# Optimization experiments

Measured on AMD Instinct MI355X. Metric: run time of the kernel, lower is better.

## Reference

```python
import jax, jax.numpy as jnp
import numpy as np

NX, NY = 8192, 8192
C1, C2, D = 2048, 2048, 512

def setup_inputs() -> dict:
    key = jax.random.key(0)
    k1, k2, k3, k4, k5 = jax.random.split(key, 5)
    scale1 = 1.0 / np.sqrt(C1)
    scale2 = 1.0 / np.sqrt(C2)
    return {
        "x": jax.random.normal(k1, (NX, C1), dtype=jnp.float32),
        "y": jax.random.normal(k2, (NY, C2), dtype=jnp.float32),
        "Wq": jax.random.uniform(k3, (D, C1), dtype=jnp.float32, minval=-scale1, maxval=scale1),
        "Wk": jax.random.uniform(k4, (D, C2), dtype=jnp.float32, minval=-scale2, maxval=scale2),
        "Wv": jax.random.uniform(k5, (D, C2), dtype=jnp.float32, minval=-scale2, maxval=scale2),
    }

def reference(x, y, Wq, Wk, Wv):
    d = Wq.shape[0]
    q = x @ Wq.T                      # [nx, d]
    k = y @ Wk.T                      # [ny, d]
    v = y @ Wv.T                      # [ny, d]
    a = (q @ k.T) * (d ** -0.5)       # [nx, ny]
    # torch.triu(ones) masks upper triangle INCLUDING diagonal -> zero where j >= i
    nx, ny = a.shape
    i = jnp.arange(nx)[:, None]
    j = jnp.arange(ny)[None, :]
    a = jnp.where(j >= i, 0.0, a)
    return a @ v                      # [nx, d]
```

## Files before the change

### kernel.cpp

```cpp
#include <hip/hip_runtime.h>
#include <hip/hip_bf16.h>


typedef __bf16 bf16x8 __attribute__((ext_vector_type(8)));
typedef __bf16 bf16x4 __attribute__((ext_vector_type(4)));
typedef float f32x4 __attribute__((ext_vector_type(4)));

#define MFMA16(a, b, c) __builtin_amdgcn_mfma_f32_16x16x32_bf16(a, b, c, 0, 0, 0)

constexpr float SCALE = 0.04419417382415922f;

__device__ __forceinline__ void ld16(const void* g, void* l) {
    __builtin_amdgcn_global_load_lds(
        (__attribute__((address_space(1))) void*)g,
        (__attribute__((address_space(3))) void*)l, 16, 0, 0);
}

__device__ __forceinline__ bf16x8 frag(const __bf16* base, int r, int c) {
    return *(const bf16x8*)((const char*)base + r * 128 + ((c ^ (r & 7)) * 16));
}

__device__ inline bf16x8 pack8(float4 a, float4 b) {
    bf16x8 r;
    r[0] = (__bf16)a.x; r[1] = (__bf16)a.y; r[2] = (__bf16)a.z; r[3] = (__bf16)a.w;
    r[4] = (__bf16)b.x; r[5] = (__bf16)b.y; r[6] = (__bf16)b.z; r[7] = (__bf16)b.w;
    return r;
}

__global__ __launch_bounds__(256) void convert_all(
    const float* __restrict__ x, const float* __restrict__ y,
    const float* __restrict__ wqf, const float* __restrict__ wkf,
    const float* __restrict__ wvf, __bf16* __restrict__ xb,
    __bf16* __restrict__ yb, __bf16* __restrict__ wqb,
    __bf16* __restrict__ wkb, __bf16* __restrict__ wvb)
{
    size_t uid = (size_t)blockIdx.x * 256 + threadIdx.x;
    const float* src; __bf16* dst; size_t off;
    if (uid < 2097152)      { src = x;   dst = xb;  off = uid; }
    else if (uid < 4194304) { src = y;   dst = yb;  off = uid - 2097152; }
    else if (uid < 4325376) { src = wqf; dst = wqb; off = uid - 4194304; }
    else if (uid < 4456448) { src = wkf; dst = wkb; off = uid - 4325376; }
    else                    { src = wvf; dst = wvb; off = uid - 4456448; }
    float4 a = ((const float4*)src)[off * 2];
    float4 b = ((const float4*)src)[off * 2 + 1];
    *(bf16x8*)(dst + off * 8) = pack8(a, b);
}

__global__ __launch_bounds__(256, 3) void gemm_qkv_bf16(
    const __bf16* __restrict__ xb, const __bf16* __restrict__ yb,
    const __bf16* __restrict__ wq, const __bf16* __restrict__ wk,
    const __bf16* __restrict__ wv, __bf16* __restrict__ qo,
    __bf16* __restrict__ ko, __bf16* __restrict__ vo)
{
    constexpr int K = 2048, N = 512;
    __shared__ __align__(16) __bf16 As[128][64];
    __shared__ __align__(16) __bf16 Bs[128][64];

    const int z = blockIdx.z;
    const __bf16* A = (z == 0) ? xb : yb;
    const __bf16* B = (z == 0) ? wq : (z == 1) ? wk : wv;
    __bf16* C = (z == 0) ? qo : (z == 1) ? ko : vo;
    const float mul = (z == 0) ? SCALE : 1.0f;

    const int tid  = threadIdx.x;
    const int wave = tid >> 6, lane = tid & 63;
    const int fr = lane & 15, fq = lane >> 4;
    const int m0 = blockIdx.x * 128, n0 = blockIdx.y * 128;
    const int wr = (wave >> 1) * 64, wc = (wave & 1) * 64;
    const int lr = lane >> 3;
    const int cd = (lane & 7) ^ lr;

    f32x4 acc[4][4];
#pragma unroll
    for (int a = 0; a < 4; ++a)
#pragma unroll
        for (int b = 0; b < 4; ++b) acc[a][b] = f32x4{0.f, 0.f, 0.f, 0.f};

    const __bf16* ag = A + (size_t)(m0 + wave * 32 + lr) * K + cd * 8;
    const __bf16* bg = B + (size_t)(n0 + wave * 32 + lr) * K + cd * 8;
    __bf16* al = &As[wave * 32][0];
    __bf16* bl = &Bs[wave * 32][0];

    for (int kk = 0; kk < K; kk += 64) {
        __syncthreads();
#pragma unroll
        for (int u = 0; u < 4; ++u) {
            ld16(ag + (size_t)(u * 8) * K + kk, al + u * 512);
            ld16(bg + (size_t)(u * 8) * K + kk, bl + u * 512);
        }
        __syncthreads();
#pragma unroll
        for (int ks = 0; ks < 2; ++ks) {
            bf16x8 af[4], bf[4];
#pragma unroll
            for (int rt = 0; rt < 4; ++rt)
                af[rt] = frag(&As[0][0], wr + rt * 16 + fr, ks * 4 + fq);
#pragma unroll
            for (int nt = 0; nt < 4; ++nt)
                bf[nt] = frag(&Bs[0][0], wc + nt * 16 + fr, ks * 4 + fq);
#pragma unroll
            for (int rt = 0; rt < 4; ++rt)
#pragma unroll
                for (int nt = 0; nt < 4; ++nt)
                    acc[rt][nt] = MFMA16(af[rt], bf[nt], acc[rt][nt]);
        }
    }

#pragma unroll
    for (int rt = 0; rt < 4; ++rt)
#pragma unroll
        for (int nt = 0; nt < 4; ++nt) {
            const int col = n0 + wc + nt * 16 + fr;
#pragma unroll
            for (int r = 0; r < 4; ++r) {
                const int row = m0 + wr + rt * 16 + fq * 4 + r;
                C[(size_t)row * N + col] = (__bf16)(acc[rt][nt][r] * mul);
            }
        }
}

__global__ __launch_bounds__(256) void transpose_v(
    const ushort* __restrict__ v, ushort* __restrict__ vT)
{
    __shared__ ushort tile[64][72];
    const int t = threadIdx.x;
    const int r0 = blockIdx.x * 64;
    const int c0 = blockIdx.y * 64;
    const int lr = t >> 2;
    const int lc = (t & 3) * 16;

    union { float4 f[2]; ushort s[16]; } u;
    const float4* vp = (const float4*)(v + (size_t)(r0 + lr) * 512 + c0 + lc);
    u.f[0] = vp[0];
    u.f[1] = vp[1];
#pragma unroll
    for (int e = 0; e < 16; ++e) tile[lc + e][lr] = u.s[e];
    __syncthreads();
    float4* op = (float4*)(vT + (size_t)(c0 + lr) * 8192 + r0 + lc);
    op[0] = *(const float4*)&tile[lr][lc];
    op[1] = *(const float4*)&tile[lr][lc + 8];
}

__global__ __launch_bounds__(256, 3) void h_gemm(
    const __bf16* __restrict__ vT, const __bf16* __restrict__ kT,
    __bf16* __restrict__ Ht)
{
    __shared__ __align__(16) __bf16 As[128][64];
    __shared__ __align__(16) __bf16 Bs[128][64];

    const int c  = blockIdx.y;
    const int m0 = (blockIdx.x & 3) * 128;
    const int n0 = (blockIdx.x >> 2) * 128;

    const int tid  = threadIdx.x;
    const int wave = tid >> 6, lane = tid & 63;
    const int fr = lane & 15, fq = lane >> 4;
    const int wr = (wave >> 1) * 64, wc = (wave & 1) * 64;
    const int lr = lane >> 3;
    const int cd = (lane & 7) ^ lr;

    f32x4 acc[4][4];
#pragma unroll
    for (int a = 0; a < 4; ++a)
#pragma unroll
        for (int b = 0; b < 4; ++b) acc[a][b] = f32x4{0.f, 0.f, 0.f, 0.f};

    const __bf16* ag = vT + (size_t)(m0 + wave * 32 + lr) * 8192 + c * 128 + cd * 8;
    const __bf16* bg = kT + (size_t)(n0 + wave * 32 + lr) * 8192 + c * 128 + cd * 8;
    __bf16* al = &As[wave * 32][0];
    __bf16* bl = &Bs[wave * 32][0];

    for (int kk = 0; kk < 128; kk += 64) {
        __syncthreads();
#pragma unroll
        for (int u = 0; u < 4; ++u) {
            ld16(ag + (size_t)(u * 8) * 8192 + kk, al + u * 512);
            ld16(bg + (size_t)(u * 8) * 8192 + kk, bl + u * 512);
        }
        __syncthreads();
#pragma unroll
        for (int ks = 0; ks < 2; ++ks) {
            bf16x8 af[4], bf[4];
#pragma unroll
            for (int rt = 0; rt < 4; ++rt)
                af[rt] = frag(&As[0][0], wr + rt * 16 + fr, ks * 4 + fq);
#pragma unroll
            for (int nt = 0; nt < 4; ++nt)
                bf[nt] = frag(&Bs[0][0], wc + nt * 16 + fr, ks * 4 + fq);
#pragma unroll
            for (int rt = 0; rt < 4; ++rt)
#pragma unroll
                for (int nt = 0; nt < 4; ++nt)
                    acc[rt][nt] = MFMA16(af[rt], bf[nt], acc[rt][nt]);
        }
    }

    __bf16* tp = Ht + (size_t)c * 262144;
#pragma unroll
    for (int rt = 0; rt < 4; ++rt)
#pragma unroll
        for (int nt = 0; nt < 4; ++nt) {
            const int col = n0 + wc + nt * 16 + fr;
#pragma unroll
            for (int r = 0; r < 4; ++r) {
                const int row = m0 + wr + rt * 16 + fq * 4 + r;
                tp[(size_t)row * 512 + col] = (__bf16)acc[rt][nt][r];
            }
        }
}

__global__ __launch_bounds__(256) void prefix_scan(
    const __bf16* __restrict__ Ht, __bf16* __restrict__ Pt)
{
    const size_t e = ((size_t)blockIdx.x * 256 + threadIdx.x) * 4;
    float a0 = 0.f, a1 = 0.f, a2 = 0.f, a3 = 0.f;
#pragma unroll 7
    for (int c = 0; c < 63; ++c) {
        bf16x4 h = *(const bf16x4*)(Ht + (size_t)c * 262144 + e);
        a0 += (float)h[0]; a1 += (float)h[1];
        a2 += (float)h[2]; a3 += (float)h[3];
        bf16x4 p;
        p[0] = (__bf16)a0; p[1] = (__bf16)a1;
        p[2] = (__bf16)a2; p[3] = (__bf16)a3;
        *(bf16x4*)(Pt + (size_t)(c + 1) * 262144 + e) = p;
    }
}

__global__ __launch_bounds__(256) void out_gemm(
    const __bf16* __restrict__ q, const __bf16* __restrict__ k,
    const __bf16* __restrict__ vT, const __bf16* __restrict__ Pt,
    float* __restrict__ out)
{
    __shared__ __align__(16) __bf16 As[128][64];
    __shared__ __align__(16) __bf16 Bs[128][64];
    __shared__ __align__(16) __bf16 Ss[128][136];

    const int t  = blockIdx.x;
    const int n0 = blockIdx.y * 128;

    const int tid  = threadIdx.x;
    const int wave = tid >> 6, lane = tid & 63;
    const int fr = lane & 15, fq = lane >> 4;
    const int wr = (wave >> 1) * 64, wc = (wave & 1) * 64;
    const int lr = lane >> 3;
    const int cd = (lane & 7) ^ lr;

    f32x4 acc[4][4];
#pragma unroll
    for (int a = 0; a < 4; ++a)
#pragma unroll
        for (int b = 0; b < 4; ++b) acc[a][b] = f32x4{0.f, 0.f, 0.f, 0.f};

    const __bf16* ag = q + (size_t)(t * 128 + wave * 32 + lr) * 512 + cd * 8;
    const __bf16* bg = k + (size_t)(t * 128 + wave * 32 + lr) * 512 + cd * 8;
    __bf16* al = &As[wave * 32][0];
    __bf16* bl = &Bs[wave * 32][0];

    for (int kk = 0; kk < 512; kk += 64) {
        __syncthreads();
#pragma unroll
        for (int u = 0; u < 4; ++u) {
            ld16(ag + (size_t)(u * 8) * 512 + kk, al + u * 512);
            ld16(bg + (size_t)(u * 8) * 512 + kk, bl + u * 512);
        }
        __syncthreads();
#pragma unroll
        for (int ks = 0; ks < 2; ++ks) {
            bf16x8 af[4], bf[4];
#pragma unroll
            for (int rt = 0; rt < 4; ++rt)
                af[rt] = frag(&As[0][0], wr + rt * 16 + fr, ks * 4 + fq);
#pragma unroll
            for (int nt = 0; nt < 4; ++nt)
                bf[nt] = frag(&Bs[0][0], wc + nt * 16 + fr, ks * 4 + fq);
#pragma unroll
            for (int rt = 0; rt < 4; ++rt)
#pragma unroll
                for (int nt = 0; nt < 4; ++nt)
                    acc[rt][nt] = MFMA16(af[rt], bf[nt], acc[rt][nt]);
        }
    }

#pragma unroll
    for (int rt = 0; rt < 4; ++rt)
#pragma unroll
        for (int nt = 0; nt < 4; ++nt) {
            const int col = wc + nt * 16 + fr;
#pragma unroll
            for (int r = 0; r < 4; ++r) {
                const int row = wr + rt * 16 + fq * 4 + r;
                float vv = (col < row) ? acc[rt][nt][r] : 0.f;
                Ss[row][col] = (__bf16)vv;
            }
            acc[rt][nt] = f32x4{0.f, 0.f, 0.f, 0.f};
        }

    if (t > 0) {
        const __bf16* bg2 = Pt + (size_t)t * 262144
                          + (size_t)(n0 + wave * 32 + lr) * 512 + cd * 8;
        for (int kk = 0; kk < 512; kk += 64) {
            __syncthreads();
#pragma unroll
            for (int u = 0; u < 4; ++u) {
                ld16(ag + (size_t)(u * 8) * 512 + kk, al + u * 512);
                ld16(bg2 + (size_t)(u * 8) * 512 + kk, bl + u * 512);
            }
            __syncthreads();
#pragma unroll
            for (int ks = 0; ks < 2; ++ks) {
                bf16x8 af[4], bf[4];
#pragma unroll
                for (int rt = 0; rt < 4; ++rt)
                    af[rt] = frag(&As[0][0], wr + rt * 16 + fr, ks * 4 + fq);
#pragma unroll
                for (int nt = 0; nt < 4; ++nt)
                    bf[nt] = frag(&Bs[0][0], wc + nt * 16 + fr, ks * 4 + fq);
#pragma unroll
                for (int rt = 0; rt < 4; ++rt)
#pragma unroll
                    for (int nt = 0; nt < 4; ++nt)
                        acc[rt][nt] = MFMA16(af[rt], bf[nt], acc[rt][nt]);
            }
        }
    }

    const __bf16* bg3 = vT + (size_t)(n0 + wave * 32 + lr) * 8192
                      + t * 128 + cd * 8;
    for (int kk = 0; kk < 128; kk += 64) {
        __syncthreads();
#pragma unroll
        for (int u = 0; u < 4; ++u)
            ld16(bg3 + (size_t)(u * 8) * 8192 + kk, bl + u * 512);
        __syncthreads();
#pragma unroll
        for (int ks = 0; ks < 2; ++ks) {
            bf16x8 af[4], bf[4];
#pragma unroll
            for (int rt = 0; rt < 4; ++rt)
                af[rt] = *(const bf16x8*)(&Ss[wr + rt * 16 + fr]
                                            [kk + ks * 32 + fq * 8]);
#pragma unroll
            for (int nt = 0; nt < 4; ++nt)
                bf[nt] = frag(&Bs[0][0], wc + nt * 16 + fr, ks * 4 + fq);
#pragma unroll
            for (int rt = 0; rt < 4; ++rt)
#pragma unroll
                for (int nt = 0; nt < 4; ++nt)
                    acc[rt][nt] = MFMA16(af[rt], bf[nt], acc[rt][nt]);
        }
    }

#pragma unroll
    for (int rt = 0; rt < 4; ++rt)
#pragma unroll
        for (int nt = 0; nt < 4; ++nt) {
            const int col = n0 + wc + nt * 16 + fr;
#pragma unroll
            for (int r = 0; r < 4; ++r) {
                const int row = t * 128 + wr + rt * 16 + fq * 4 + r;
                out[(size_t)row * 512 + col] = acc[rt][nt][r];
            }
        }
}

extern "C" void kernel_launch(void* const* d_in, const int* in_sizes, int n_in,
                              void* d_out, int out_size, void* d_ws, size_t ws_size,
                              hipStream_t stream) {
    const float* x  = (const float*)d_in[0];
    const float* y  = (const float*)d_in[1];
    const float* Wq = (const float*)d_in[2];
    const float* Wk = (const float*)d_in[3];
    const float* Wv = (const float*)d_in[4];
    float* out = (float*)d_out;

    const size_t QK = (size_t)8192 * 512;
    __bf16* q  = (__bf16*)d_ws;
    __bf16* k  = q + QK;
    __bf16* v  = k + QK;
    __bf16* vT = v + QK;
    __bf16* xb  = vT + QK;
    __bf16* yb  = xb + 16777216;
    __bf16* wqb = yb + 16777216;
    __bf16* wkb = wqb + 1048576;
    __bf16* wvb = wkb + 1048576;
    __bf16* kT = v;
    __bf16* Ht = xb;
    __bf16* Pt = yb;

    convert_all<<<17920, 256, 0, stream>>>(x, y, Wq, Wk, Wv, xb, yb, wqb, wkb, wvb);
    gemm_qkv_bf16<<<dim3(64, 4, 3), 256, 0, stream>>>(xb, yb, wqb, wkb, wvb, q, k, v);
    transpose_v<<<dim3(128, 8), 256, 0, stream>>>((const ushort*)v, (ushort*)vT);
    transpose_v<<<dim3(128, 8), 256, 0, stream>>>((const ushort*)k, (ushort*)kT);
    h_gemm<<<dim3(16, 63), 256, 0, stream>>>(vT, kT, Ht);
    prefix_scan<<<256, 256, 0, stream>>>(Ht, Pt);
    out_gemm<<<dim3(64, 4), 256, 0, stream>>>(q, k, vT, Pt, out);
}
```

Before: 278.5 us.

## Precompute masked diagonal score blocks once and coalesce fp32-to-bf16 conversion

The masked diagonal q·kᵀ block is moved out of out_gemm into a separate s_diag kernel that computes it once per row tile and writes it to workspace. Previously each of the 4 column-block CTAs recomputed it. out_gemm then loads the block via async LDS loads, drops the large Ss shared buffer, and gains a 3-blocks-per-CU occupancy hint. The conversion kernel is also rewritten so each wave reads contiguous float4s and writes 8-byte bf16 chunks for better coalescing. The cost is an extra launch and a global round-trip for the diagonal blocks.

```diff
diff --git a/kernel.cpp b/kernel.cpp
--- a/kernel.cpp
+++ b/kernel.cpp
@@ -20,10 +20,10 @@
     return *(const bf16x8*)((const char*)base + r * 128 + ((c ^ (r & 7)) * 16));
 }
 
-__device__ inline bf16x8 pack8(float4 a, float4 b) {
-    bf16x8 r;
-    r[0] = (__bf16)a.x; r[1] = (__bf16)a.y; r[2] = (__bf16)a.z; r[3] = (__bf16)a.w;
-    r[4] = (__bf16)b.x; r[5] = (__bf16)b.y; r[6] = (__bf16)b.z; r[7] = (__bf16)b.w;
+__device__ inline bf16x4 pack4(float4 a) {
+    bf16x4 r;
+    r[0] = (__bf16)a.x; r[1] = (__bf16)a.y;
+    r[2] = (__bf16)a.z; r[3] = (__bf16)a.w;
     return r;
 }
 
@@ -34,16 +34,22 @@
     __bf16* __restrict__ yb, __bf16* __restrict__ wqb,
     __bf16* __restrict__ wkb, __bf16* __restrict__ wvb)
 {
-    size_t uid = (size_t)blockIdx.x * 256 + threadIdx.x;
-    const float* src; __bf16* dst; size_t off;
-    if (uid < 2097152)      { src = x;   dst = xb;  off = uid; }
-    else if (uid < 4194304) { src = y;   dst = yb;  off = uid - 2097152; }
-    else if (uid < 4325376) { src = wqf; dst = wqb; off = uid - 4194304; }
-    else if (uid < 4456448) { src = wkf; dst = wkb; off = uid - 4325376; }
-    else                    { src = wvf; dst = wvb; off = uid - 4456448; }
-    float4 a = ((const float4*)src)[off * 2];
-    float4 b = ((const float4*)src)[off * 2 + 1];
-    *(bf16x8*)(dst + off * 8) = pack8(a, b);
+    const size_t tid = (size_t)blockIdx.x * 256 + threadIdx.x;
+    const size_t w = tid >> 6;
+    const int lane = (int)(tid & 63);
+    size_t f = w * 512;
+    const float* src; __bf16* dst;
+    if (f < 16777216)      { src = x;   dst = xb;  }
+    else if (f < 33554432) { src = y;   dst = yb;  f -= 16777216; }
+    else if (f < 34603008) { src = wqf; dst = wqb; f -= 33554432; }
+    else if (f < 35651584) { src = wkf; dst = wkb; f -= 34603008; }
+    else                   { src = wvf; dst = wvb; f -= 35651584; }
+    const float4* s4 = (const float4*)(src + f);
+    float4 a = s4[lane];
+    float4 b = s4[64 + lane];
+    __bf16* d = dst + f;
+    *(bf16x4*)(d + lane * 4)       = pack4(a);
+    *(bf16x4*)(d + 256 + lane * 4) = pack4(b);
 }
 
 __global__ __launch_bounds__(256, 3) void gemm_qkv_bf16(
@@ -226,17 +232,15 @@
     }
 }
 
-__global__ __launch_bounds__(256) void out_gemm(
+__global__ __launch_bounds__(256, 3) void s_diag(
     const __bf16* __restrict__ q, const __bf16* __restrict__ k,
-    const __bf16* __restrict__ vT, const __bf16* __restrict__ Pt,
-    float* __restrict__ out)
-{
+    __bf16* __restrict__ Sd)
+{
+    constexpr int K = 512;
     __shared__ __align__(16) __bf16 As[128][64];
     __shared__ __align__(16) __bf16 Bs[128][64];
-    __shared__ __align__(16) __bf16 Ss[128][136];
-
-    const int t  = blockIdx.x;
-    const int n0 = blockIdx.y * 128;
+
+    const int t = blockIdx.x;
 
     const int tid  = threadIdx.x;
     const int wave = tid >> 6, lane = tid & 63;
@@ -251,17 +255,17 @@
 #pragma unroll
         for (int b = 0; b < 4; ++b) acc[a][b] = f32x4{0.f, 0.f, 0.f, 0.f};
 
-    const __bf16* ag = q + (size_t)(t * 128 + wave * 32 + lr) * 512 + cd * 8;
-    const __bf16* bg = k + (size_t)(t * 128 + wave * 32 + lr) * 512 + cd * 8;
+    const __bf16* ag = q + (size_t)(t * 128 + wave * 32 + lr) * K + cd * 8;
+    const __bf16* bg = k + (size_t)(t * 128 + wave * 32 + lr) * K + cd * 8;
     __bf16* al = &As[wave * 32][0];
     __bf16* bl = &Bs[wave * 32][0];
 
-    for (int kk = 0; kk < 512; kk += 64) {
+    for (int kk = 0; kk < K; kk += 64) {
         __syncthreads();
 #pragma unroll
         for (int u = 0; u < 4; ++u) {
-            ld16(ag + (size_t)(u * 8) * 512 + kk, al + u * 512);
-            ld16(bg + (size_t)(u * 8) * 512 + kk, bl + u * 512);
+            ld16(ag + (size_t)(u * 8) * K + kk, al + u * 512);
+            ld16(bg + (size_t)(u * 8) * K + kk, bl + u * 512);
         }
         __syncthreads();
 #pragma unroll
@@ -281,6 +285,7 @@
         }
     }
 
+    __bf16* tp = Sd + (size_t)t * 16384;
 #pragma unroll
     for (int rt = 0; rt < 4; ++rt)
 #pragma unroll
@@ -290,14 +295,43 @@
             for (int r = 0; r < 4; ++r) {
                 const int row = wr + rt * 16 + fq * 4 + r;
                 float vv = (col < row) ? acc[rt][nt][r] : 0.f;
-                Ss[row][col] = (__bf16)vv;
-            }
-            acc[rt][nt] = f32x4{0.f, 0.f, 0.f, 0.f};
-        }
+                tp[row * 128 + col] = (__bf16)vv;
+            }
+        }
+}
+
+__global__ __launch_bounds__(256, 3) void out_gemm(
+    const __bf16* __restrict__ q, const __bf16* __restrict__ Sd,
+    const __bf16* __restrict__ vT, const __bf16* __restrict__ Pt,
+    float* __restrict__ out)
+{
+    __shared__ __align__(16) __bf16 As[128][64];
+    __shared__ __align__(16) __bf16 Bs[128][64];
+
+    const int t  = blockIdx.x;
+    const int n0 = blockIdx.y * 128;
+
+    const int tid  = threadIdx.x;
+    const int wave = tid >> 6, lane = tid & 63;
+    const int fr = lane & 15, fq = lane >> 4;
+    const int wr = (wave >> 1) * 64, wc = (wave & 1) * 64;
+    const int lr = lane >> 3;
+    const int cd = (lane & 7) ^ lr;
+    const int srow = wave * 32 + lr;
+
+    f32x4 acc[4][4];
+#pragma unroll
+    for (int a = 0; a < 4; ++a)
+#pragma unroll
+        for (int b = 0; b < 4; ++b) acc[a][b] = f32x4{0.f, 0.f, 0.f, 0.f};
+
+    __bf16* al = &As[wave * 32][0];
+    __bf16* bl = &Bs[wave * 32][0];
 
     if (t > 0) {
+        const __bf16* ag = q + (size_t)(t * 128 + srow) * 512 + cd * 8;
         const __bf16* bg2 = Pt + (size_t)t * 262144
-                          + (size_t)(n0 + wave * 32 + lr) * 512 + cd * 8;
+                          + (size_t)(n0 + srow) * 512 + cd * 8;
         for (int kk = 0; kk < 512; kk += 64) {
             __syncthreads();
 #pragma unroll
@@ -324,21 +358,22 @@
         }
     }
 
-    const __bf16* bg3 = vT + (size_t)(n0 + wave * 32 + lr) * 8192
-                      + t * 128 + cd * 8;
+    const __bf16* at3 = Sd + (size_t)t * 16384 + (size_t)srow * 128 + cd * 8;
+    const __bf16* bg3 = vT + (size_t)(n0 + srow) * 8192 + t * 128 + cd * 8;
     for (int kk = 0; kk < 128; kk += 64) {
         __syncthreads();
 #pragma unroll
-        for (int u = 0; u < 4; ++u)
+        for (int u = 0; u < 4; ++u) {
+            ld16(at3 + (size_t)(u * 8) * 128 + kk, al + u * 512);
             ld16(bg3 + (size_t)(u * 8) * 8192 + kk, bl + u * 512);
+        }
         __syncthreads();
 #pragma unroll
         for (int ks = 0; ks < 2; ++ks) {
             bf16x8 af[4], bf[4];
 #pragma unroll
             for (int rt = 0; rt < 4; ++rt)
-                af[rt] = *(const bf16x8*)(&Ss[wr + rt * 16 + fr]
-                                            [kk + ks * 32 + fq * 8]);
+                af[rt] = frag(&As[0][0], wr + rt * 16 + fr, ks * 4 + fq);
 #pragma unroll
             for (int nt = 0; nt < 4; ++nt)
                 bf[nt] = frag(&Bs[0][0], wc + nt * 16 + fr, ks * 4 + fq);
@@ -386,12 +421,14 @@
     __bf16* kT = v;
     __bf16* Ht = xb;
     __bf16* Pt = yb;
+    __bf16* Sd = wqb;
 
     convert_all<<<17920, 256, 0, stream>>>(x, y, Wq, Wk, Wv, xb, yb, wqb, wkb, wvb);
     gemm_qkv_bf16<<<dim3(64, 4, 3), 256, 0, stream>>>(xb, yb, wqb, wkb, wvb, q, k, v);
     transpose_v<<<dim3(128, 8), 256, 0, stream>>>((const ushort*)v, (ushort*)vT);
     transpose_v<<<dim3(128, 8), 256, 0, stream>>>((const ushort*)k, (ushort*)kT);
     h_gemm<<<dim3(16, 63), 256, 0, stream>>>(vT, kT, Ht);
+    s_diag<<<64, 256, 0, stream>>>(q, k, Sd);
     prefix_scan<<<256, 256, 0, stream>>>(Ht, Pt);
-    out_gemm<<<dim3(64, 4), 256, 0, stream>>>(q, k, vT, Pt, out);
-}
+    out_gemm<<<dim3(64, 4), 256, 0, stream>>>(q, Sd, vT, Pt, out);
+}
```

Measured after the change: 278.0 us. No clear change (-0.2%).
